# Kernel optimization log

Measured on AMD Instinct MI355X. Metric: run time of the kernel, lower is better.

The kernel has to match this reference:

```python
import jax, jax.numpy as jnp
import numpy as np

TOP_K = 2  # config.n_expert_capacity


def setup_inputs() -> dict:
    key = jax.random.key(0)
    k1, k2, k3, k4 = jax.random.split(key, 4)
    B, S, D, F, E = 2, 2048, 1024, 4096, 8
    x = jax.random.normal(k1, (B, S, D), dtype=jnp.float32)
    # kaiming-ish scaling so router logits / activations stay well-conditioned
    choice = jax.random.normal(k2, (E, D), dtype=jnp.float32) / np.sqrt(D)
    W1 = jax.random.normal(k3, (E, D, F), dtype=jnp.float32) / np.sqrt(D)
    W2 = jax.random.normal(k4, (E, F, D), dtype=jnp.float32) / np.sqrt(F)
    return {"x": x, "choice": choice, "W1": W1, "W2": W2}


def reference(x, choice, W1, W2):
    B, S, D = x.shape
    E = choice.shape[0]
    # Router: softmax over experts, then top-k (weights NOT renormalized, per source)
    logits = jnp.einsum('bsd,ed->bse', x, choice)          # [B,S,E]
    weights = jax.nn.softmax(logits, axis=-1)
    k_w, k_idx = jax.lax.top_k(weights, TOP_K)             # [B,S,K]
    # Dense combine weights: zero for non-selected experts -> same math as scatter/gather
    cw = jnp.sum(jax.nn.one_hot(k_idx, E, dtype=x.dtype) * k_w[..., None], axis=-2)  # [B,S,E]
    xt = x.reshape(B * S, D)
    cwt = cw.reshape(B * S, E)
    y = jnp.zeros_like(xt)
    for e in range(E):  # small fixed expert loop; avoids [T,E,F] intermediate
        h = jax.nn.silu(xt @ W1[e]) @ W2[e]                # [T,D]
        y = y + cwt[:, e:e+1] * h
    # dropout p=0.0 / eval mode -> identity
    return y.reshape(B, S, D)
```

## Files before the change

### kernel.cpp

```cpp
#include <hip/hip_runtime.h>
#include <hip/hip_fp16.h>
#include <cmath>

#define T_TOKENS 4096
#define DDIM     1024
#define FDIM     4096
#define NEXP     8
#define NPAIR    8192
#define MBMAX    64

typedef _Float16 half8  __attribute__((ext_vector_type(8)));
typedef _Float16 half4v __attribute__((ext_vector_type(4)));
typedef float    floatx4 __attribute__((ext_vector_type(4)));

#define GLOAD16(g, l) __builtin_amdgcn_global_load_lds(                     \
    (const __attribute__((address_space(1))) void*)(g),                      \
    (__attribute__((address_space(3))) void*)(l), 16, 0, 0)

static const size_t OFF_XH  = 0;
static const size_t SZ_XH   = (size_t)T_TOKENS * DDIM * 2;
static const size_t OFF_W1T = OFF_XH + SZ_XH;
static const size_t SZ_WT   = (size_t)NEXP * FDIM * DDIM * 2;
static const size_t OFF_W2T = OFF_W1T + SZ_WT;
static const size_t OFF_H   = OFF_W2T + SZ_WT;
static const size_t SZ_H    = (size_t)NPAIR * FDIM * 2;
static const size_t OFF_PT  = OFF_H + SZ_H;
static const size_t OFF_PW  = OFF_PT + NPAIR * 4;
static const size_t OFF_TI  = OFF_PW + NPAIR * 4;
static const size_t OFF_TW  = OFF_TI + NPAIR * 4;
static const size_t OFF_CNT = OFF_TW + NPAIR * 4;
static const size_t OFF_OFS = OFF_CNT + 64;
static const size_t OFF_CUR = OFF_OFS + 64;
static const size_t WS_NEED = OFF_CUR + 64;

__global__ __launch_bounds__(256)
void router_kernel(const float* __restrict__ x, const float* __restrict__ choice,
                   _Float16* __restrict__ xh, int* __restrict__ top_idx,
                   float* __restrict__ top_w, int* __restrict__ counts)
{
    __shared__ float ch[NEXP * DDIM];
    for (int i = threadIdx.x * 4; i < NEXP * DDIM; i += 256 * 4) {
        *(float4*)&ch[i] = *(const float4*)&choice[i];
    }
    __syncthreads();

    const int lane = threadIdx.x & 63;
    const int wv   = threadIdx.x >> 6;
    const int t    = blockIdx.x * 4 + wv;

    const float* xp = x + (size_t)t * DDIM;
    float4 xr[4];
#pragma unroll
    for (int p = 0; p < 4; ++p) xr[p] = *(const float4*)(xp + p * 256 + lane * 4);

#pragma unroll
    for (int p = 0; p < 4; ++p) {
        half4v hv = { (_Float16)xr[p].x, (_Float16)xr[p].y,
                      (_Float16)xr[p].z, (_Float16)xr[p].w };
        *(half4v*)(xh + (size_t)t * DDIM + p * 256 + lane * 4) = hv;
    }

    float lg[NEXP];
#pragma unroll
    for (int e = 0; e < NEXP; ++e) {
        float s = 0.f;
#pragma unroll
        for (int p = 0; p < 4; ++p) {
            float4 c4 = *(float4*)&ch[e * DDIM + p * 256 + lane * 4];
            s += xr[p].x * c4.x + xr[p].y * c4.y + xr[p].z * c4.z + xr[p].w * c4.w;
        }
#pragma unroll
        for (int o = 32; o; o >>= 1) s += __shfl_xor(s, o, 64);
        lg[e] = s;
    }

    if (lane == 0) {
        float mx = lg[0];
#pragma unroll
        for (int e = 1; e < NEXP; ++e) mx = fmaxf(mx, lg[e]);
        float w[NEXP]; float sum = 0.f;
#pragma unroll
        for (int e = 0; e < NEXP; ++e) { w[e] = expf(lg[e] - mx); sum += w[e]; }
        float inv = 1.f / sum;
#pragma unroll
        for (int e = 0; e < NEXP; ++e) w[e] *= inv;
        int i0 = 0; float w0 = w[0];
#pragma unroll
        for (int e = 1; e < NEXP; ++e) if (w[e] > w0) { w0 = w[e]; i0 = e; }
        int i1 = -1; float w1 = -1.f;
#pragma unroll
        for (int e = 0; e < NEXP; ++e) if (e != i0 && w[e] > w1) { w1 = w[e]; i1 = e; }
        top_idx[t * 2 + 0] = i0;  top_w[t * 2 + 0] = w0;
        top_idx[t * 2 + 1] = i1;  top_w[t * 2 + 1] = w1;
        atomicAdd(&counts[i0], 1);
        atomicAdd(&counts[i1], 1);
    }
}

__global__ void scan_kernel(const int* __restrict__ counts, int* __restrict__ offsets,
                            int* __restrict__ cursors)
{
    if (threadIdx.x == 0) {
        int o = 0;
        for (int e = 0; e < NEXP; ++e) { offsets[e] = o; cursors[e] = o; o += counts[e]; }
        offsets[NEXP] = o;
    }
}

__global__ __launch_bounds__(256)
void fill_kernel(const int* __restrict__ top_idx, const float* __restrict__ top_w,
                 int* __restrict__ cursors, int* __restrict__ pair_tok,
                 float* __restrict__ pair_w)
{
    int t = blockIdx.x * 256 + threadIdx.x;
#pragma unroll
    for (int k = 0; k < 2; ++k) {
        int e = top_idx[t * 2 + k];
        int pos = atomicAdd(&cursors[e], 1);
        pair_tok[pos] = t;
        pair_w[pos]   = top_w[t * 2 + k];
    }
}

__global__ __launch_bounds__(256)
void transpose_cvt(const float* __restrict__ in, _Float16* __restrict__ out, int R, int C)
{
    __shared__ float tile[64][65];
    const int e  = blockIdx.z;
    const float*    ip = in  + ((size_t)e * R + blockIdx.y * 64) * C + blockIdx.x * 64;
    _Float16*       op = out + ((size_t)e * C + blockIdx.x * 64) * R + blockIdx.y * 64;
    const int lr = threadIdx.x >> 4;
    const int lc = (threadIdx.x & 15) * 4;
#pragma unroll
    for (int p = 0; p < 4; ++p) {
        float4 v = *(const float4*)(ip + (size_t)(lr + p * 16) * C + lc);
        tile[lc + 0][lr + p * 16] = v.x;
        tile[lc + 1][lr + p * 16] = v.y;
        tile[lc + 2][lr + p * 16] = v.z;
        tile[lc + 3][lr + p * 16] = v.w;
    }
    __syncthreads();
#pragma unroll
    for (int p = 0; p < 4; ++p) {
        int oc = lr + p * 16;
        half4v hv = { (_Float16)tile[oc][lc + 0], (_Float16)tile[oc][lc + 1],
                      (_Float16)tile[oc][lc + 2], (_Float16)tile[oc][lc + 3] };
        *(half4v*)(op + (size_t)oc * R + lc) = hv;
    }
}

template<bool GATHER, int EPI, int GM>
__global__ __launch_bounds__(256)
void moe_gemm(const _Float16* __restrict__ Abase, const _Float16* __restrict__ Bt,
              _Float16* __restrict__ Hout, float* __restrict__ Yout,
              const int* __restrict__ pair_tok, const float* __restrict__ pair_w,
              const int* __restrict__ counts, const int* __restrict__ offsets,
              const int K, const int N, const int NB)
{
    const int q  = gridDim.x >> 3;
    const int wg = (blockIdx.x & 7) * q + (blockIdx.x >> 3);
    const int per_e = MBMAX * NB;
    const int e  = wg / per_e;
    int ide = wg - e * per_e;
    const int g = ide / (NB * GM);
    ide -= g * (NB * GM);
    const int nb  = ide / GM;
    const int mb  = g * GM + (ide - nb * GM);

    const int cnt = counts[e];
    if (mb * 128 >= cnt) return;
    const int off = offsets[e];

    const int tid  = threadIdx.x;
    const int lane = tid & 63;
    const int wv   = tid >> 6;
    const int wm   = wv >> 1, wn = wv & 1;

    __shared__ __align__(16) _Float16 As[128 * 64];
    __shared__ __align__(16) _Float16 Bs[128 * 64];

    const int crow = lane >> 3;
    const int kofs = (lane & 7) * 8;

    const _Float16* asrc[4];
    const _Float16* bsrc[4];
#pragma unroll
    for (int i = 0; i < 4; ++i) {
        const int ca = wv * 4 + i;
        int r = mb * 128 + ca * 8 + crow;
        int pr = off + (r < cnt ? r : cnt - 1);
        long rowi = GATHER ? (long)pair_tok[pr] : (long)pr;
        asrc[i] = Abase + (size_t)rowi * K + kofs;
        const int n = nb * 128 + ca * 8 + crow;
        bsrc[i] = Bt + ((size_t)e * N + n) * K + kofs;
    }

    floatx4 acc[4][4] = {};
    const int kc = (lane >> 4) * 8;
    const int fr = lane & 15;
    const int nK = K >> 6;

    for (int kt = 0; kt < nK; ++kt) {
        __syncthreads();
        const int ko = kt * 64;
#pragma unroll
        for (int i = 0; i < 4; ++i) {
            GLOAD16(asrc[i] + ko, &As[(wv * 4 + i) * 512]);
            GLOAD16(bsrc[i] + ko, &Bs[(wv * 4 + i) * 512]);
        }
        __syncthreads();
#pragma unroll
        for (int s = 0; s < 2; ++s) {
            half8 af[4], bf[4];
#pragma unroll
            for (int i = 0; i < 4; ++i)
                af[i] = *(const half8*)&As[(wm * 64 + i * 16 + fr) * 64 + s * 32 + kc];
#pragma unroll
            for (int j = 0; j < 4; ++j)
                bf[j] = *(const half8*)&Bs[(wn * 64 + j * 16 + fr) * 64 + s * 32 + kc];
#pragma unroll
            for (int i = 0; i < 4; ++i)
#pragma unroll
                for (int j = 0; j < 4; ++j)
                    acc[i][j] = __builtin_amdgcn_mfma_f32_16x16x32_f16(af[i], bf[j], acc[i][j], 0, 0, 0);
        }
    }

    const int qr = lane >> 4;
    const int nbase = nb * 128 + wn * 64;
#pragma unroll
    for (int i = 0; i < 4; ++i) {
#pragma unroll
        for (int r = 0; r < 4; ++r) {
            const int gm = mb * 128 + wm * 64 + i * 16 + qr * 4 + r;
            if (gm < cnt) {
                if (EPI == 0) {
                    const size_t hrow = (size_t)(off + gm) * FDIM;
#pragma unroll
                    for (int j = 0; j < 4; ++j) {
                        float v = acc[i][j][r];
                        v = v / (1.f + expf(-v));
                        Hout[hrow + nbase + j * 16 + fr] = (_Float16)v;
                    }
                } else {
                    const int pr = off + gm;
                    const int tok = pair_tok[pr];
                    const float w = pair_w[pr];
                    const size_t yrow = (size_t)tok * DDIM;
#pragma unroll
                    for (int j = 0; j < 4; ++j)
                        atomicAdd(&Yout[yrow + nbase + j * 16 + fr], w * acc[i][j][r]);
                }
            }
        }
    }
}

extern "C" void kernel_launch(void* const* d_in, const int* in_sizes, int n_in,
                              void* d_out, int out_size, void* d_ws, size_t ws_size,
                              hipStream_t stream)
{
    const float* x      = (const float*)d_in[0];
    const float* choice = (const float*)d_in[1];
    const float* W1     = (const float*)d_in[2];
    const float* W2     = (const float*)d_in[3];
    float* y = (float*)d_out;

    char* ws = (char*)d_ws;
    if (ws_size < WS_NEED) return;

    _Float16* xh  = (_Float16*)(ws + OFF_XH);
    _Float16* W1T = (_Float16*)(ws + OFF_W1T);
    _Float16* W2T = (_Float16*)(ws + OFF_W2T);
    _Float16* H   = (_Float16*)(ws + OFF_H);
    int*   pair_tok = (int*)(ws + OFF_PT);
    float* pair_w   = (float*)(ws + OFF_PW);
    int*   top_idx  = (int*)(ws + OFF_TI);
    float* top_w    = (float*)(ws + OFF_TW);
    int*   counts   = (int*)(ws + OFF_CNT);
    int*   offsets  = (int*)(ws + OFF_OFS);
    int*   cursors  = (int*)(ws + OFF_CUR);

    hipMemsetAsync(counts, 0, 192, stream);
    hipMemsetAsync(d_out, 0, (size_t)T_TOKENS * DDIM * 4, stream);

    router_kernel<<<T_TOKENS / 4, 256, 0, stream>>>(x, choice, xh, top_idx, top_w, counts);
    scan_kernel<<<1, 64, 0, stream>>>(counts, offsets, cursors);
    fill_kernel<<<T_TOKENS / 256, 256, 0, stream>>>(top_idx, top_w, cursors, pair_tok, pair_w);

    transpose_cvt<<<dim3(FDIM / 64, DDIM / 64, NEXP), 256, 0, stream>>>(W1, W1T, DDIM, FDIM);
    transpose_cvt<<<dim3(DDIM / 64, FDIM / 64, NEXP), 256, 0, stream>>>(W2, W2T, FDIM, DDIM);

    const int NB1 = FDIM / 128;
    moe_gemm<true, 0, 64><<<NEXP * MBMAX * NB1, 256, 0, stream>>>(
        xh, W1T, H, nullptr, pair_tok, pair_w, counts, offsets, DDIM, FDIM, NB1);

    const int NB2 = DDIM / 128;
    moe_gemm<false, 1, 2><<<NEXP * MBMAX * NB2, 256, 0, stream>>>(
        H, W2T, nullptr, y, pair_tok, pair_w, counts, offsets, FDIM, DDIM, NB2);
}
```

Before: 846.1 us.

## Double-buffer MoE GEMM LDS, swizzle tiles, replace atomic scatter with combine kernel

The MoE GEMM now double-buffers its A and B LDS tiles, prefetching the next K slice while MFMAs run on the current one. It also XOR-swizzles the LDS layout to avoid bank conflicts on fragment reads. The grid becomes a fixed, persistent-style set of m-blocks that loop over an expert's row tiles, instead of launching up to 64 blocks per expert and exiting early. The second GEMM writes per-pair fp32 rows into a buffer that reuses the W1T region, and a new combine kernel does the weighted sum of each token's two expert rows. This removes the output memset and the fp32 atomics, at the cost of an extra 32 MB write and read plus one more launch.

```diff
diff --git a/kernel.cpp b/kernel.cpp
--- a/kernel.cpp
+++ b/kernel.cpp
@@ -7,7 +7,6 @@
 #define FDIM     4096
 #define NEXP     8
 #define NPAIR    8192
-#define MBMAX    64
 
 typedef _Float16 half8  __attribute__((ext_vector_type(8)));
 typedef _Float16 half4v __attribute__((ext_vector_type(4)));
@@ -25,10 +24,10 @@
 static const size_t OFF_H   = OFF_W2T + SZ_WT;
 static const size_t SZ_H    = (size_t)NPAIR * FDIM * 2;
 static const size_t OFF_PT  = OFF_H + SZ_H;
-static const size_t OFF_PW  = OFF_PT + NPAIR * 4;
-static const size_t OFF_TI  = OFF_PW + NPAIR * 4;
+static const size_t OFF_TI  = OFF_PT + NPAIR * 4;
 static const size_t OFF_TW  = OFF_TI + NPAIR * 4;
-static const size_t OFF_CNT = OFF_TW + NPAIR * 4;
+static const size_t OFF_PS  = OFF_TW + NPAIR * 4;
+static const size_t OFF_CNT = OFF_PS + NPAIR * 4;
 static const size_t OFF_OFS = OFF_CNT + 64;
 static const size_t OFF_CUR = OFF_OFS + 64;
 static const size_t WS_NEED = OFF_CUR + 64;
@@ -110,7 +109,7 @@
 __global__ __launch_bounds__(256)
 void fill_kernel(const int* __restrict__ top_idx, const float* __restrict__ top_w,
                  int* __restrict__ cursors, int* __restrict__ pair_tok,
-                 float* __restrict__ pair_w)
+                 int* __restrict__ pslot)
 {
     int t = blockIdx.x * 256 + threadIdx.x;
 #pragma unroll
@@ -118,7 +117,7 @@
         int e = top_idx[t * 2 + k];
         int pos = atomicAdd(&cursors[e], 1);
         pair_tok[pos] = t;
-        pair_w[pos]   = top_w[t * 2 + k];
+        pslot[t * 2 + k] = pos;
     }
 }
 
@@ -149,26 +148,26 @@
     }
 }
 
-template<bool GATHER, int EPI, int GM>
+template<bool GATHER, int EPI, int GM, int NB>
 __global__ __launch_bounds__(256)
 void moe_gemm(const _Float16* __restrict__ Abase, const _Float16* __restrict__ Bt,
-              _Float16* __restrict__ Hout, float* __restrict__ Yout,
-              const int* __restrict__ pair_tok, const float* __restrict__ pair_w,
+              _Float16* __restrict__ Hout, float* __restrict__ H2out,
+              const int* __restrict__ pair_tok,
               const int* __restrict__ counts, const int* __restrict__ offsets,
-              const int K, const int N, const int NB)
-{
+              const int K, const int N)
+{
+    const int MBSTR = 16;
     const int q  = gridDim.x >> 3;
     const int wg = (blockIdx.x & 7) * q + (blockIdx.x >> 3);
-    const int per_e = MBMAX * NB;
+    const int per_e = MBSTR * NB;
     const int e  = wg / per_e;
     int ide = wg - e * per_e;
     const int g = ide / (NB * GM);
     ide -= g * (NB * GM);
     const int nb  = ide / GM;
-    const int mb  = g * GM + (ide - nb * GM);
+    const int mb0 = g * GM + (ide - nb * GM);
 
     const int cnt = counts[e];
-    if (mb * 128 >= cnt) return;
     const int off = offsets[e];
 
     const int tid  = threadIdx.x;
@@ -176,84 +175,114 @@
     const int wv   = tid >> 6;
     const int wm   = wv >> 1, wn = wv & 1;
 
-    __shared__ __align__(16) _Float16 As[128 * 64];
-    __shared__ __align__(16) _Float16 Bs[128 * 64];
+    __shared__ __align__(16) _Float16 As[2][128 * 64];
+    __shared__ __align__(16) _Float16 Bs[2][128 * 64];
 
     const int crow = lane >> 3;
-    const int kofs = (lane & 7) * 8;
-
-    const _Float16* asrc[4];
-    const _Float16* bsrc[4];
-#pragma unroll
-    for (int i = 0; i < 4; ++i) {
-        const int ca = wv * 4 + i;
-        int r = mb * 128 + ca * 8 + crow;
-        int pr = off + (r < cnt ? r : cnt - 1);
-        long rowi = GATHER ? (long)pair_tok[pr] : (long)pr;
-        asrc[i] = Abase + (size_t)rowi * K + kofs;
-        const int n = nb * 128 + ca * 8 + crow;
-        bsrc[i] = Bt + ((size_t)e * N + n) * K + kofs;
-    }
-
-    floatx4 acc[4][4] = {};
+    const int swz  = ((lane & 7) * 8) ^ (crow << 3);
+
     const int kc = (lane >> 4) * 8;
     const int fr = lane & 15;
+    const int rsw = (fr & 7) << 3;
     const int nK = K >> 6;
 
-    for (int kt = 0; kt < nK; ++kt) {
+    const _Float16* bsrc[4];
+#pragma unroll
+    for (int i = 0; i < 4; ++i) {
+        const int n = nb * 128 + (wv * 4 + i) * 8 + crow;
+        bsrc[i] = Bt + ((size_t)e * N + n) * K + swz;
+    }
+
+    for (int mb = mb0; mb * 128 < cnt; mb += MBSTR) {
+        const _Float16* asrc[4];
+#pragma unroll
+        for (int i = 0; i < 4; ++i) {
+            int r = mb * 128 + (wv * 4 + i) * 8 + crow;
+            int pr = off + (r < cnt ? r : cnt - 1);
+            long rowi = GATHER ? (long)pair_tok[pr] : (long)pr;
+            asrc[i] = Abase + (size_t)rowi * K + swz;
+        }
+
+        floatx4 acc[4][4] = {};
+
+#pragma unroll
+        for (int i = 0; i < 4; ++i) {
+            GLOAD16(asrc[i], &As[0][(wv * 4 + i) * 512]);
+            GLOAD16(bsrc[i], &Bs[0][(wv * 4 + i) * 512]);
+        }
         __syncthreads();
-        const int ko = kt * 64;
-#pragma unroll
-        for (int i = 0; i < 4; ++i) {
-            GLOAD16(asrc[i] + ko, &As[(wv * 4 + i) * 512]);
-            GLOAD16(bsrc[i] + ko, &Bs[(wv * 4 + i) * 512]);
-        }
-        __syncthreads();
-#pragma unroll
-        for (int s = 0; s < 2; ++s) {
-            half8 af[4], bf[4];
-#pragma unroll
-            for (int i = 0; i < 4; ++i)
-                af[i] = *(const half8*)&As[(wm * 64 + i * 16 + fr) * 64 + s * 32 + kc];
-#pragma unroll
-            for (int j = 0; j < 4; ++j)
-                bf[j] = *(const half8*)&Bs[(wn * 64 + j * 16 + fr) * 64 + s * 32 + kc];
-#pragma unroll
-            for (int i = 0; i < 4; ++i)
-#pragma unroll
-                for (int j = 0; j < 4; ++j)
-                    acc[i][j] = __builtin_amdgcn_mfma_f32_16x16x32_f16(af[i], bf[j], acc[i][j], 0, 0, 0);
-        }
-    }
-
-    const int qr = lane >> 4;
-    const int nbase = nb * 128 + wn * 64;
-#pragma unroll
-    for (int i = 0; i < 4; ++i) {
-#pragma unroll
-        for (int r = 0; r < 4; ++r) {
-            const int gm = mb * 128 + wm * 64 + i * 16 + qr * 4 + r;
-            if (gm < cnt) {
-                if (EPI == 0) {
-                    const size_t hrow = (size_t)(off + gm) * FDIM;
-#pragma unroll
-                    for (int j = 0; j < 4; ++j) {
-                        float v = acc[i][j][r];
-                        v = v / (1.f + expf(-v));
-                        Hout[hrow + nbase + j * 16 + fr] = (_Float16)v;
-                    }
-                } else {
-                    const int pr = off + gm;
-                    const int tok = pair_tok[pr];
-                    const float w = pair_w[pr];
-                    const size_t yrow = (size_t)tok * DDIM;
-#pragma unroll
-                    for (int j = 0; j < 4; ++j)
-                        atomicAdd(&Yout[yrow + nbase + j * 16 + fr], w * acc[i][j][r]);
+
+        int cur = 0;
+        for (int kt = 0; kt < nK; ++kt) {
+            if (kt + 1 < nK) {
+                const int ko = (kt + 1) * 64;
+#pragma unroll
+                for (int i = 0; i < 4; ++i) {
+                    GLOAD16(asrc[i] + ko, &As[cur ^ 1][(wv * 4 + i) * 512]);
+                    GLOAD16(bsrc[i] + ko, &Bs[cur ^ 1][(wv * 4 + i) * 512]);
                 }
             }
-        }
-    }
+#pragma unroll
+            for (int s = 0; s < 2; ++s) {
+                const int rc = (s * 32 + kc) ^ rsw;
+                half8 af[4], bf[4];
+#pragma unroll
+                for (int i = 0; i < 4; ++i)
+                    af[i] = *(const half8*)&As[cur][(wm * 64 + i * 16 + fr) * 64 + rc];
+#pragma unroll
+                for (int j = 0; j < 4; ++j)
+                    bf[j] = *(const half8*)&Bs[cur][(wn * 64 + j * 16 + fr) * 64 + rc];
+#pragma unroll
+                for (int i = 0; i < 4; ++i)
+#pragma unroll
+                    for (int j = 0; j < 4; ++j)
+                        acc[i][j] = __builtin_amdgcn_mfma_f32_16x16x32_f16(af[i], bf[j], acc[i][j], 0, 0, 0);
+            }
+            __syncthreads();
+            cur ^= 1;
+        }
+
+        const int qr = lane >> 4;
+        const int nbase = nb * 128 + wn * 64;
+#pragma unroll
+        for (int i = 0; i < 4; ++i) {
+#pragma unroll
+            for (int r = 0; r < 4; ++r) {
+                const int gm = mb * 128 + wm * 64 + i * 16 + qr * 4 + r;
+                if (gm < cnt) {
+                    if (EPI == 0) {
+                        const size_t hrow = (size_t)(off + gm) * FDIM;
+#pragma unroll
+                        for (int j = 0; j < 4; ++j) {
+                            float v = acc[i][j][r];
+                            v = v / (1.f + expf(-v));
+                            Hout[hrow + nbase + j * 16 + fr] = (_Float16)v;
+                        }
+                    } else {
+                        const size_t hrow = (size_t)(off + gm) * DDIM;
+#pragma unroll
+                        for (int j = 0; j < 4; ++j)
+                            H2out[hrow + nbase + j * 16 + fr] = acc[i][j][r];
+                    }
+                }
+            }
+        }
+    }
+}
+
+__global__ __launch_bounds__(256)
+void combine_kernel(const float* __restrict__ H2, const int* __restrict__ pslot,
+                    const float* __restrict__ top_w, float* __restrict__ y)
+{
+    const int t  = blockIdx.x;
+    const int p0 = pslot[t * 2 + 0], p1 = pslot[t * 2 + 1];
+    const float w0 = top_w[t * 2 + 0], w1 = top_w[t * 2 + 1];
+    const int d = threadIdx.x * 4;
+    float4 a = *(const float4*)&H2[(size_t)p0 * DDIM + d];
+    float4 b = *(const float4*)&H2[(size_t)p1 * DDIM + d];
+    float4 o = { w0 * a.x + w1 * b.x, w0 * a.y + w1 * b.y,
+                 w0 * a.z + w1 * b.z, w0 * a.w + w1 * b.w };
+    *(float4*)&y[(size_t)t * DDIM + d] = o;
 }
 
 extern "C" void kernel_launch(void* const* d_in, const int* in_sizes, int n_in,
@@ -273,29 +302,29 @@
     _Float16* W1T = (_Float16*)(ws + OFF_W1T);
     _Float16* W2T = (_Float16*)(ws + OFF_W2T);
     _Float16* H   = (_Float16*)(ws + OFF_H);
+    float*    H2  = (float*)(ws + OFF_W1T);
     int*   pair_tok = (int*)(ws + OFF_PT);
-    float* pair_w   = (float*)(ws + OFF_PW);
     int*   top_idx  = (int*)(ws + OFF_TI);
     float* top_w    = (float*)(ws + OFF_TW);
+    int*   pslot    = (int*)(ws + OFF_PS);
     int*   counts   = (int*)(ws + OFF_CNT);
     int*   offsets  = (int*)(ws + OFF_OFS);
     int*   cursors  = (int*)(ws + OFF_CUR);
 
     hipMemsetAsync(counts, 0, 192, stream);
-    hipMemsetAsync(d_out, 0, (size_t)T_TOKENS * DDIM * 4, stream);
 
     router_kernel<<<T_TOKENS / 4, 256, 0, stream>>>(x, choice, xh, top_idx, top_w, counts);
     scan_kernel<<<1, 64, 0, stream>>>(counts, offsets, cursors);
-    fill_kernel<<<T_TOKENS / 256, 256, 0, stream>>>(top_idx, top_w, cursors, pair_tok, pair_w);
+    fill_kernel<<<T_TOKENS / 256, 256, 0, stream>>>(top_idx, top_w, cursors, pair_tok, pslot);
 
     transpose_cvt<<<dim3(FDIM / 64, DDIM / 64, NEXP), 256, 0, stream>>>(W1, W1T, DDIM, FDIM);
     transpose_cvt<<<dim3(DDIM / 64, FDIM / 64, NEXP), 256, 0, stream>>>(W2, W2T, FDIM, DDIM);
 
-    const int NB1 = FDIM / 128;
-    moe_gemm<true, 0, 64><<<NEXP * MBMAX * NB1, 256, 0, stream>>>(
-        xh, W1T, H, nullptr, pair_tok, pair_w, counts, offsets, DDIM, FDIM, NB1);
-
-    const int NB2 = DDIM / 128;
-    moe_gemm<false, 1, 2><<<NEXP * MBMAX * NB2, 256, 0, stream>>>(
-        H, W2T, nullptr, y, pair_tok, pair_w, counts, offsets, FDIM, DDIM, NB2);
-}
+    moe_gemm<true, 0, 16, FDIM / 128><<<NEXP * 16 * (FDIM / 128), 256, 0, stream>>>(
+        xh, W1T, H, nullptr, pair_tok, counts, offsets, DDIM, FDIM);
+
+    moe_gemm<false, 1, 2, DDIM / 128><<<NEXP * 16 * (DDIM / 128), 256, 0, stream>>>(
+        H, W2T, nullptr, H2, pair_tok, counts, offsets, FDIM, DDIM);
+
+    combine_kernel<<<T_TOKENS, 256, 0, stream>>>(H2, pslot, top_w, y);
+}
```

Result: faster. 766.3 us (-9.4%).
